# Kernel optimization log

Measured on AMD Instinct MI355X. Metric: run time of the kernel, lower is better.

## Reference

```python
import jax, jax.numpy as jnp
import numpy as np

HEADS = 4
LOCAL_CTX = 8  # local_attn_ctx (stride)


def _strided_transpose(x, n_ctx, local_ctx):
    # [B, n_ctx, E] -> reshape [B, n_ctx//local, local, E] -> swap -> [B, n_ctx, E]
    B, _, E = x.shape
    bT = n_ctx // local_ctx
    return x.reshape(B, bT, local_ctx, E).transpose(0, 2, 1, 3).reshape(B, n_ctx, E)


def _strided_untranspose(a, n_ctx, local_ctx):
    B, _, E = a.shape
    bT = n_ctx // local_ctx
    return a.reshape(B, local_ctx, bT, E).transpose(0, 2, 1, 3).reshape(B, n_ctx, E)


def setup_inputs() -> dict:
    key = jax.random.key(0)
    ks = jax.random.split(key, 6)
    B, T, E = 2048, 64, 256
    value = jax.random.normal(ks[0], (B, T, E), dtype=jnp.float32)
    k_in = jax.random.normal(ks[1], (B, T, E), dtype=jnp.float32)
    query = jax.random.normal(ks[2], (B, T, E), dtype=jnp.float32)
    mask = jnp.ones((B, T), dtype=jnp.int32)  # unused by the block
    W_ff = jax.random.normal(ks[3], (256, T * E), dtype=jnp.float32) * (1.0 / np.sqrt(T * E))
    b_ff = jax.random.normal(ks[4], (256,), dtype=jnp.float32) * 0.01
    return {"value": value, "key": k_in, "query": query, "mask": mask, "W_ff": W_ff, "b_ff": b_ff}


def reference(value, key, query, mask, W_ff, b_ff):
    B, n_ctx, E = query.shape
    # strided transpose of q, k, v
    q = _strided_transpose(query, n_ctx, LOCAL_CTX)
    k = _strided_transpose(key, n_ctx, LOCAL_CTX)
    v = _strided_transpose(value, n_ctx, LOCAL_CTX)
    scale = 1.0 / np.sqrt(E // HEADS)  # n_state = embd // heads
    w = jax.nn.softmax(jnp.einsum('bqe,bke->bqk', q, k) * scale, axis=-1)
    a = jnp.einsum('bqk,bke->bqe', w, v)
    attention = _strided_untranspose(a, n_ctx, LOCAL_CTX)
    # residual + dropout (eval-mode identity)
    x = attention + query
    # flatten-linear + ReLU
    out = jax.nn.relu(x.reshape(B, n_ctx * E) @ W_ff.T + b_ff)
    return (out, attention)
```

## Files before the change

### kernel.cpp

```cpp
#include <hip/hip_runtime.h>
#include <stdint.h>

typedef __attribute__((ext_vector_type(8))) short s16x8;
typedef __attribute__((ext_vector_type(8))) _Float16 h16x8;
typedef __attribute__((ext_vector_type(4))) float f32x4;

__device__ __forceinline__ unsigned short f2h_bits(float f) {
  union { _Float16 h; unsigned short u; } cv;
  cv.h = (_Float16)f;
  return cv.u;
}
__device__ __forceinline__ f32x4 mfma16h(h16x8 a, h16x8 b, f32x4 c) {
  return __builtin_amdgcn_mfma_f32_16x16x32_f16(a, b, c, 0, 0, 0);
}

typedef const unsigned int __attribute__((address_space(1)))* as1_u32p;
typedef unsigned int __attribute__((address_space(3)))* as3_u32p;
__device__ __forceinline__ void async_ld16(const void* g, void* l) {
  __builtin_amdgcn_global_load_lds((as1_u32p)g, (as3_u32p)l, 16, 0, 0);
}

__device__ __forceinline__ void stage_kq(char* buf, const float* Kb, int qi,
                                         int w, int lane) {
#pragma unroll
  for (int i = 0; i < 4; ++i) {
    int seg = w * 4 + i;
    int row = seg * 4 + (lane >> 4);
    int sg = (lane & 15) ^ (row & 7);
    async_ld16(Kb + row * 256 + qi * 64 + sg * 4, buf + seg * 1024);
  }
}

__device__ __forceinline__ void qk_quarter(const char* buf, const float* Qb, int qi,
                                           int w, int n, int q, f32x4* accS) {
#pragma unroll
  for (int kkl = 0; kkl < 2; ++kkl) {
    const float* qsrc = Qb + (16 * w + n) * 256 + qi * 64 + kkl * 32 + q * 8;
    float4 q0 = *(const float4*)qsrc;
    float4 q1 = *(const float4*)(qsrc + 4);
    h16x8 qh;
    qh[0] = (_Float16)q0.x; qh[1] = (_Float16)q0.y;
    qh[2] = (_Float16)q0.z; qh[3] = (_Float16)q0.w;
    qh[4] = (_Float16)q1.x; qh[5] = (_Float16)q1.y;
    qh[6] = (_Float16)q1.z; qh[7] = (_Float16)q1.w;
    const int g = kkl * 8 + q * 2;
#pragma unroll
    for (int c = 0; c < 4; ++c) {
      int row = 16 * c + n;
      int s = row & 7;
      float4 k0 = *(const float4*)(buf + row * 256 + ((g ^ s) * 16));
      float4 k1 = *(const float4*)(buf + row * 256 + (((g + 1) ^ s) * 16));
      h16x8 kh;
      kh[0] = (_Float16)k0.x; kh[1] = (_Float16)k0.y;
      kh[2] = (_Float16)k0.z; kh[3] = (_Float16)k0.w;
      kh[4] = (_Float16)k1.x; kh[5] = (_Float16)k1.y;
      kh[6] = (_Float16)k1.z; kh[7] = (_Float16)k1.w;
      accS[c] = mfma16h(qh, kh, accS[c]);
    }
  }
}

__device__ __forceinline__ void write_vq(char* base, int e, int tg, const float2* g) {
  s16x8 lo, hi;
#pragma unroll
  for (int j = 0; j < 8; ++j) {
    lo[j] = (short)f2h_bits(g[j].x);
    hi[j] = (short)f2h_bits(g[j].y);
  }
  int sw = ((e >> 1) & 7) << 4;
  *(s16x8*)(base + e * 128 + ((16 * tg) ^ sw)) = lo;
  *(s16x8*)(base + (e + 1) * 128 + ((16 * tg) ^ sw)) = hi;
}

__global__ __launch_bounds__(256, 2) void attn_kernel(
    const float* __restrict__ Vg, const float* __restrict__ Kg,
    const float* __restrict__ Qg, float* __restrict__ attn_out,
    unsigned short* __restrict__ xb ) {
  __shared__ __align__(16) char smem[65536];
  char* b0 = smem;
  char* b1 = smem + 16384;
  char* Vt = smem + 32768;
  char* PLB = smem;

  const int b = blockIdx.x;
  const int tid = threadIdx.x;
  const int lane = tid & 63;
  const int w = tid >> 6;
  const int n = lane & 15;
  const int q = lane >> 4;

  const float* Qb = Qg + (size_t)b * 64 * 256;
  const float* Kb = Kg + (size_t)b * 64 * 256;
  const float* Vb = Vg + (size_t)b * 64 * 256;

  const int ep2 = (tid & 31) * 2;
  const int tg = tid >> 5;

  f32x4 accS[4];
#pragma unroll
  for (int c = 0; c < 4; ++c) accS[c] = f32x4{0.f, 0.f, 0.f, 0.f};

  stage_kq(b0, Kb, 0, w, lane);
  stage_kq(b1, Kb, 1, w, lane);
  float2 g0[8], g1[8];
#pragma unroll
  for (int j = 0; j < 8; ++j) g0[j] = *(const float2*)(Vb + (tg * 8 + j) * 256 + 0 + ep2);
#pragma unroll
  for (int j = 0; j < 8; ++j) g1[j] = *(const float2*)(Vb + (tg * 8 + j) * 256 + 64 + ep2);
  __syncthreads();

  write_vq(Vt, 0 + ep2, tg, g0);
  write_vq(Vt, 64 + ep2, tg, g1);
  float2 g2[8], g3[8];
#pragma unroll
  for (int j = 0; j < 8; ++j) g2[j] = *(const float2*)(Vb + (tg * 8 + j) * 256 + 128 + ep2);
#pragma unroll
  for (int j = 0; j < 8; ++j) g3[j] = *(const float2*)(Vb + (tg * 8 + j) * 256 + 192 + ep2);

  qk_quarter(b0, Qb, 0, w, n, q, accS);
  __syncthreads();
  stage_kq(b0, Kb, 2, w, lane);
  qk_quarter(b1, Qb, 1, w, n, q, accS);
  __syncthreads();
  stage_kq(b1, Kb, 3, w, lane);
  write_vq(Vt, 128 + ep2, tg, g2);
  write_vq(Vt, 192 + ep2, tg, g3);
  qk_quarter(b0, Qb, 2, w, n, q, accS);
  __syncthreads();
  qk_quarter(b1, Qb, 3, w, n, q, accS);

  const float scale = 0.125f;
  float p[4][4];
#pragma unroll
  for (int r = 0; r < 4; ++r) {
    float m = -1e30f;
#pragma unroll
    for (int c = 0; c < 4; ++c) m = fmaxf(m, accS[c][r]);
#pragma unroll
    for (int mk = 1; mk < 16; mk <<= 1) m = fmaxf(m, __shfl_xor(m, mk, 64));
    float s = 0.f;
#pragma unroll
    for (int c = 0; c < 4; ++c) {
      float e = __expf((accS[c][r] - m) * scale);
      p[c][r] = e;
      s += e;
    }
#pragma unroll
    for (int mk = 1; mk < 16; mk <<= 1) s += __shfl_xor(s, mk, 64);
    float inv = 1.0f / s;
#pragma unroll
    for (int c = 0; c < 4; ++c) p[c][r] *= inv;
  }

#pragma unroll
  for (int r = 0; r < 4; ++r) {
    int row = 16 * w + 4 * q + r;
    int sw = (row & 7) << 4;
#pragma unroll
    for (int c = 0; c < 4; ++c)
      *(unsigned short*)(PLB + row * 128 + ((2 * (16 * c + n)) ^ sw)) =
          f2h_bits(p[c][r]);
  }

  __syncthreads();

  f32x4 accA[4];
#pragma unroll
  for (int qi = 0; qi < 4; ++qi) {
#pragma unroll
    for (int c = 0; c < 4; ++c) accA[c] = f32x4{0.f, 0.f, 0.f, 0.f};
    __builtin_amdgcn_s_setprio(1);
#pragma unroll
    for (int ks = 0; ks < 2; ++ks) {
      const int cb = (ks * 32 + q * 8) * 2;
      h16x8 af = *(const h16x8*)(PLB + (16 * w + n) * 128 + (cb ^ ((n & 7) << 4)));
#pragma unroll
      for (int c = 0; c < 4; ++c) {
        int row = qi * 64 + 16 * c + n;
        h16x8 bf = *(const h16x8*)(Vt + row * 128 + (cb ^ (((row >> 1) & 7) << 4)));
        accA[c] = mfma16h(af, bf, accA[c]);
      }
    }
    __builtin_amdgcn_s_setprio(0);

#pragma unroll
    for (int r = 0; r < 4; ++r) {
      int t = 16 * w + 4 * q + r;
      const float* qrow = Qb + t * 256 + qi * 64;
      size_t base = ((size_t)b * 64 + t) * 256 + qi * 64;
#pragma unroll
      for (int c = 0; c < 4; ++c) {
        int e = 16 * c + n;
        float aval = accA[c][r];
        attn_out[base + e] = aval;
        if (xb) xb[base + e] = f2h_bits(aval + qrow[e]);
      }
    }
  }
}

__global__ __launch_bounds__(256) void w2b_kernel(const float* __restrict__ W,
                                                  unsigned short* __restrict__ Wb) {
  int i = blockIdx.x * 256 + threadIdx.x;
  float4 v = ((const float4*)W)[i];
  ushort4 o;
  o.x = f2h_bits(v.x); o.y = f2h_bits(v.y); o.z = f2h_bits(v.z); o.w = f2h_bits(v.w);
  ((ushort4*)Wb)[i] = o;
}

template <bool USE_XB>
__global__ __launch_bounds__(256) void ff_kernel(
    const unsigned short* __restrict__ xb, const float* __restrict__ attn,
    const float* __restrict__ query, const unsigned short* __restrict__ Wb,
    float* __restrict__ part, int kchunk) {
  __shared__ __align__(16) unsigned short As[64 * 72];
  __shared__ __align__(16) unsigned short Bs[64 * 72];
  const int tid = threadIdx.x;
  const int lane = tid & 63, w = tid >> 6, n = lane & 15, q = lane >> 4;
  const int m0 = blockIdx.x * 64;
  const int n0 = blockIdx.y * 64;
  const int k0 = blockIdx.z * kchunk;

  f32x4 acc[4];
#pragma unroll
  for (int c = 0; c < 4; ++c) acc[c] = f32x4{0.f, 0.f, 0.f, 0.f};

  const int srow = tid >> 3;
  const int scol = (tid & 7) * 8;

  for (int kk = 0; kk < kchunk; kk += 64) {
#pragma unroll
    for (int rr = 0; rr < 2; ++rr) {
      int row = rr * 32 + srow;
      size_t ga = (size_t)(m0 + row) * 16384 + k0 + kk + scol;
      if (USE_XB) {
        *(uint4*)(As + row * 72 + scol) = *(const uint4*)(xb + ga);
      } else {
        float4 a0 = *(const float4*)(attn + ga);
        float4 a1 = *(const float4*)(attn + ga + 4);
        float4 q0 = *(const float4*)(query + ga);
        float4 q1 = *(const float4*)(query + ga + 4);
        ushort4 h0, h1;
        h0.x = f2h_bits(a0.x + q0.x); h0.y = f2h_bits(a0.y + q0.y);
        h0.z = f2h_bits(a0.z + q0.z); h0.w = f2h_bits(a0.w + q0.w);
        h1.x = f2h_bits(a1.x + q1.x); h1.y = f2h_bits(a1.y + q1.y);
        h1.z = f2h_bits(a1.z + q1.z); h1.w = f2h_bits(a1.w + q1.w);
        *(ushort4*)(As + row * 72 + scol) = h0;
        *(ushort4*)(As + row * 72 + scol + 4) = h1;
      }
      size_t gw = (size_t)(n0 + row) * 16384 + k0 + kk + scol;
      *(uint4*)(Bs + row * 72 + scol) = *(const uint4*)(Wb + gw);
    }
    __syncthreads();
#pragma unroll
    for (int ks = 0; ks < 2; ++ks) {
      const int colb = ks * 32 + q * 8;
      h16x8 af = *(const h16x8*)(As + (16 * w + n) * 72 + colb);
#pragma unroll
      for (int c = 0; c < 4; ++c) {
        h16x8 bf = *(const h16x8*)(Bs + (16 * c + n) * 72 + colb);
        acc[c] = mfma16h(af, bf, acc[c]);
      }
    }
    __syncthreads();
  }
#pragma unroll
  for (int r = 0; r < 4; ++r) {
    int m = m0 + 16 * w + 4 * q + r;
#pragma unroll
    for (int c = 0; c < 4; ++c) {
      int nn = n0 + 16 * c + n;
      part[((size_t)blockIdx.z * 2048 + m) * 256 + nn] = acc[c][r];
    }
  }
}

__global__ __launch_bounds__(256) void relu_kernel(const float* __restrict__ part,
                                                   const float* __restrict__ bias,
                                                   float* __restrict__ out, int KS) {
  int idx = blockIdx.x * 256 + threadIdx.x;
  float s = bias[idx & 255];
  for (int ks = 0; ks < KS; ++ks) s += part[(size_t)ks * 2048 * 256 + idx];
  out[idx] = fmaxf(s, 0.f);
}

extern "C" void kernel_launch(void* const* d_in, const int* in_sizes, int n_in,
                              void* d_out, int out_size, void* d_ws, size_t ws_size,
                              hipStream_t stream) {
  const float* value = (const float*)d_in[0];
  const float* key   = (const float*)d_in[1];
  const float* query = (const float*)d_in[2];
  const float* W_ff  = (const float*)d_in[4];
  const float* b_ff  = (const float*)d_in[5];

  float* out  = (float*)d_out;
  float* attn = out + (size_t)2048 * 256;

  const int KS = 4;
  const size_t wb_bytes   = (size_t)256 * 16384 * 2;
  const size_t part_bytes = (size_t)KS * 2048 * 256 * 4;
  const size_t xb_bytes   = (size_t)2048 * 64 * 256 * 2;
  unsigned short* Wb = (unsigned short*)d_ws;
  float* part = (float*)((char*)d_ws + wb_bytes);
  bool use_xb = ws_size >= wb_bytes + part_bytes + xb_bytes;
  unsigned short* xb =
      use_xb ? (unsigned short*)((char*)d_ws + wb_bytes + part_bytes) : nullptr;

  w2b_kernel<<<4096, 256, 0, stream>>>(W_ff, Wb);
  attn_kernel<<<2048, 256, 0, stream>>>(value, key, query, attn, xb);
  dim3 gb(32, 4, KS);
  if (use_xb)
    ff_kernel<true><<<gb, 256, 0, stream>>>(xb, nullptr, nullptr, Wb, part, 16384 / KS);
  else
    ff_kernel<false><<<gb, 256, 0, stream>>>(nullptr, attn, query, Wb, part, 16384 / KS);
  relu_kernel<<<2048, 256, 0, stream>>>(part, b_ff, out, KS);
}
```

Before: 280.3 us.

## Split fused attention kernel into QK-softmax and PV kernels via global P buffer

Splits the single attention kernel into a QK+softmax kernel that writes fp16 probabilities in MFMA fragment order to a workspace buffer, and a PV kernel that reloads them and stages V in LDS. K is now read straight from global memory into registers instead of through async LDS double-buffering. The aim is lower LDS use and register pressure per kernel, giving higher occupancy and simpler scheduling. In exchange it adds an extra launch, a 16 MB global round trip for P, a second read of Q in the PV kernel, and it drops the overlap of V loads with QK compute.

```diff
diff --git a/kernel.cpp b/kernel.cpp
--- a/kernel.cpp
+++ b/kernel.cpp
@@ -13,74 +13,17 @@
 __device__ __forceinline__ f32x4 mfma16h(h16x8 a, h16x8 b, f32x4 c) {
   return __builtin_amdgcn_mfma_f32_16x16x32_f16(a, b, c, 0, 0, 0);
 }
-
-typedef const unsigned int __attribute__((address_space(1)))* as1_u32p;
-typedef unsigned int __attribute__((address_space(3)))* as3_u32p;
-__device__ __forceinline__ void async_ld16(const void* g, void* l) {
-  __builtin_amdgcn_global_load_lds((as1_u32p)g, (as3_u32p)l, 16, 0, 0);
-}
-
-__device__ __forceinline__ void stage_kq(char* buf, const float* Kb, int qi,
-                                         int w, int lane) {
-#pragma unroll
-  for (int i = 0; i < 4; ++i) {
-    int seg = w * 4 + i;
-    int row = seg * 4 + (lane >> 4);
-    int sg = (lane & 15) ^ (row & 7);
-    async_ld16(Kb + row * 256 + qi * 64 + sg * 4, buf + seg * 1024);
-  }
-}
-
-__device__ __forceinline__ void qk_quarter(const char* buf, const float* Qb, int qi,
-                                           int w, int n, int q, f32x4* accS) {
-#pragma unroll
-  for (int kkl = 0; kkl < 2; ++kkl) {
-    const float* qsrc = Qb + (16 * w + n) * 256 + qi * 64 + kkl * 32 + q * 8;
-    float4 q0 = *(const float4*)qsrc;
-    float4 q1 = *(const float4*)(qsrc + 4);
-    h16x8 qh;
-    qh[0] = (_Float16)q0.x; qh[1] = (_Float16)q0.y;
-    qh[2] = (_Float16)q0.z; qh[3] = (_Float16)q0.w;
-    qh[4] = (_Float16)q1.x; qh[5] = (_Float16)q1.y;
-    qh[6] = (_Float16)q1.z; qh[7] = (_Float16)q1.w;
-    const int g = kkl * 8 + q * 2;
-#pragma unroll
-    for (int c = 0; c < 4; ++c) {
-      int row = 16 * c + n;
-      int s = row & 7;
-      float4 k0 = *(const float4*)(buf + row * 256 + ((g ^ s) * 16));
-      float4 k1 = *(const float4*)(buf + row * 256 + (((g + 1) ^ s) * 16));
-      h16x8 kh;
-      kh[0] = (_Float16)k0.x; kh[1] = (_Float16)k0.y;
-      kh[2] = (_Float16)k0.z; kh[3] = (_Float16)k0.w;
-      kh[4] = (_Float16)k1.x; kh[5] = (_Float16)k1.y;
-      kh[6] = (_Float16)k1.z; kh[7] = (_Float16)k1.w;
-      accS[c] = mfma16h(qh, kh, accS[c]);
-    }
-  }
-}
-
-__device__ __forceinline__ void write_vq(char* base, int e, int tg, const float2* g) {
-  s16x8 lo, hi;
-#pragma unroll
-  for (int j = 0; j < 8; ++j) {
-    lo[j] = (short)f2h_bits(g[j].x);
-    hi[j] = (short)f2h_bits(g[j].y);
-  }
-  int sw = ((e >> 1) & 7) << 4;
-  *(s16x8*)(base + e * 128 + ((16 * tg) ^ sw)) = lo;
-  *(s16x8*)(base + (e + 1) * 128 + ((16 * tg) ^ sw)) = hi;
-}
-
-__global__ __launch_bounds__(256, 2) void attn_kernel(
-    const float* __restrict__ Vg, const float* __restrict__ Kg,
-    const float* __restrict__ Qg, float* __restrict__ attn_out,
-    unsigned short* __restrict__ xb ) {
-  __shared__ __align__(16) char smem[65536];
-  char* b0 = smem;
-  char* b1 = smem + 16384;
-  char* Vt = smem + 32768;
-  char* PLB = smem;
+__device__ __forceinline__ h16x8 cvt8(float4 x, float4 y) {
+  h16x8 r;
+  r[0] = (_Float16)x.x; r[1] = (_Float16)x.y; r[2] = (_Float16)x.z; r[3] = (_Float16)x.w;
+  r[4] = (_Float16)y.x; r[5] = (_Float16)y.y; r[6] = (_Float16)y.z; r[7] = (_Float16)y.w;
+  return r;
+}
+
+__global__ __launch_bounds__(256) void qk_kernel(
+    const float* __restrict__ Kg, const float* __restrict__ Qg,
+    unsigned short* __restrict__ Pg) {
+  __shared__ __align__(16) char PL[8192];
 
   const int b = blockIdx.x;
   const int tid = threadIdx.x;
@@ -91,43 +34,32 @@
 
   const float* Qb = Qg + (size_t)b * 64 * 256;
   const float* Kb = Kg + (size_t)b * 64 * 256;
-  const float* Vb = Vg + (size_t)b * 64 * 256;
-
-  const int ep2 = (tid & 31) * 2;
-  const int tg = tid >> 5;
 
   f32x4 accS[4];
 #pragma unroll
   for (int c = 0; c < 4; ++c) accS[c] = f32x4{0.f, 0.f, 0.f, 0.f};
 
-  stage_kq(b0, Kb, 0, w, lane);
-  stage_kq(b1, Kb, 1, w, lane);
-  float2 g0[8], g1[8];
-#pragma unroll
-  for (int j = 0; j < 8; ++j) g0[j] = *(const float2*)(Vb + (tg * 8 + j) * 256 + 0 + ep2);
-#pragma unroll
-  for (int j = 0; j < 8; ++j) g1[j] = *(const float2*)(Vb + (tg * 8 + j) * 256 + 64 + ep2);
-  __syncthreads();
-
-  write_vq(Vt, 0 + ep2, tg, g0);
-  write_vq(Vt, 64 + ep2, tg, g1);
-  float2 g2[8], g3[8];
-#pragma unroll
-  for (int j = 0; j < 8; ++j) g2[j] = *(const float2*)(Vb + (tg * 8 + j) * 256 + 128 + ep2);
-#pragma unroll
-  for (int j = 0; j < 8; ++j) g3[j] = *(const float2*)(Vb + (tg * 8 + j) * 256 + 192 + ep2);
-
-  qk_quarter(b0, Qb, 0, w, n, q, accS);
-  __syncthreads();
-  stage_kq(b0, Kb, 2, w, lane);
-  qk_quarter(b1, Qb, 1, w, n, q, accS);
-  __syncthreads();
-  stage_kq(b1, Kb, 3, w, lane);
-  write_vq(Vt, 128 + ep2, tg, g2);
-  write_vq(Vt, 192 + ep2, tg, g3);
-  qk_quarter(b0, Qb, 2, w, n, q, accS);
-  __syncthreads();
-  qk_quarter(b1, Qb, 3, w, n, q, accS);
+#pragma unroll
+  for (int ph = 0; ph < 2; ++ph) {
+#pragma unroll
+    for (int kk = 0; kk < 4; ++kk) {
+      const int cb = ph * 128 + kk * 32 + q * 8;
+      const float* qsrc = Qb + (16 * w + n) * 256 + cb;
+      float4 q0 = *(const float4*)qsrc;
+      float4 q1 = *(const float4*)(qsrc + 4);
+      float4 k0[4], k1[4];
+#pragma unroll
+      for (int c = 0; c < 4; ++c) {
+        const float* ksrc = Kb + (16 * c + n) * 256 + cb;
+        k0[c] = *(const float4*)ksrc;
+        k1[c] = *(const float4*)(ksrc + 4);
+      }
+      h16x8 qh = cvt8(q0, q1);
+#pragma unroll
+      for (int c = 0; c < 4; ++c)
+        accS[c] = mfma16h(qh, cvt8(k0[c], k1[c]), accS[c]);
+    }
+  }
 
   const float scale = 0.125f;
   float p[4][4];
@@ -158,10 +90,64 @@
     int sw = (row & 7) << 4;
 #pragma unroll
     for (int c = 0; c < 4; ++c)
-      *(unsigned short*)(PLB + row * 128 + ((2 * (16 * c + n)) ^ sw)) =
+      *(unsigned short*)(PL + row * 128 + ((2 * (16 * c + n)) ^ sw)) =
           f2h_bits(p[c][r]);
   }
-
+#pragma unroll
+  for (int ks = 0; ks < 2; ++ks) {
+    const int cb = (ks * 32 + q * 8) * 2;
+    s16x8 af = *(const s16x8*)(PL + (16 * w + n) * 128 + (cb ^ ((n & 7) << 4)));
+    *(s16x8*)(Pg + ((size_t)(b * 4 + w) * 2 + ks) * 512 + lane * 8) = af;
+  }
+}
+
+__device__ __forceinline__ void write_vq(char* base, int e, int tg, const float2* g) {
+  s16x8 lo, hi;
+#pragma unroll
+  for (int j = 0; j < 8; ++j) {
+    lo[j] = (short)f2h_bits(g[j].x);
+    hi[j] = (short)f2h_bits(g[j].y);
+  }
+  int sw = ((e >> 1) & 7) << 4;
+  *(s16x8*)(base + e * 128 + ((16 * tg) ^ sw)) = lo;
+  *(s16x8*)(base + (e + 1) * 128 + ((16 * tg) ^ sw)) = hi;
+}
+
+__global__ __launch_bounds__(256) void pv_kernel(
+    const float* __restrict__ Vg, const float* __restrict__ Qg,
+    const unsigned short* __restrict__ Pg, float* __restrict__ attn_out,
+    unsigned short* __restrict__ xb ) {
+  __shared__ __align__(16) char Vt[32768];
+
+  const int b = blockIdx.x;
+  const int tid = threadIdx.x;
+  const int lane = tid & 63;
+  const int w = tid >> 6;
+  const int n = lane & 15;
+  const int q = lane >> 4;
+
+  const float* Vb = Vg + (size_t)b * 64 * 256;
+  const float* Qb = Qg + (size_t)b * 64 * 256;
+
+  const int ep2 = (tid & 31) * 2;
+  const int tg = tid >> 5;
+
+  float2 g0[8], g1[8], g2[8], g3[8];
+#pragma unroll
+  for (int j = 0; j < 8; ++j) g0[j] = *(const float2*)(Vb + (tg * 8 + j) * 256 + 0 + ep2);
+#pragma unroll
+  for (int j = 0; j < 8; ++j) g1[j] = *(const float2*)(Vb + (tg * 8 + j) * 256 + 64 + ep2);
+#pragma unroll
+  for (int j = 0; j < 8; ++j) g2[j] = *(const float2*)(Vb + (tg * 8 + j) * 256 + 128 + ep2);
+#pragma unroll
+  for (int j = 0; j < 8; ++j) g3[j] = *(const float2*)(Vb + (tg * 8 + j) * 256 + 192 + ep2);
+  h16x8 af0 = *(const h16x8*)(Pg + ((size_t)(b * 4 + w) * 2 + 0) * 512 + lane * 8);
+  h16x8 af1 = *(const h16x8*)(Pg + ((size_t)(b * 4 + w) * 2 + 1) * 512 + lane * 8);
+
+  write_vq(Vt, 0 + ep2, tg, g0);
+  write_vq(Vt, 64 + ep2, tg, g1);
+  write_vq(Vt, 128 + ep2, tg, g2);
+  write_vq(Vt, 192 + ep2, tg, g3);
   __syncthreads();
 
   f32x4 accA[4];
@@ -173,7 +159,7 @@
 #pragma unroll
     for (int ks = 0; ks < 2; ++ks) {
       const int cb = (ks * 32 + q * 8) * 2;
-      h16x8 af = *(const h16x8*)(PLB + (16 * w + n) * 128 + (cb ^ ((n & 7) << 4)));
+      h16x8 af = ks ? af1 : af0;
 #pragma unroll
       for (int c = 0; c < 4; ++c) {
         int row = qi * 64 + 16 * c + n;
@@ -299,18 +285,22 @@
   const int KS = 4;
   const size_t wb_bytes   = (size_t)256 * 16384 * 2;
   const size_t part_bytes = (size_t)KS * 2048 * 256 * 4;
+  const size_t p_bytes    = (size_t)2048 * 64 * 64 * 2;
   const size_t xb_bytes   = (size_t)2048 * 64 * 256 * 2;
   unsigned short* Wb = (unsigned short*)d_ws;
   float* part = (float*)((char*)d_ws + wb_bytes);
-  bool use_xb = ws_size >= wb_bytes + part_bytes + xb_bytes;
-  unsigned short* xb =
-      use_xb ? (unsigned short*)((char*)d_ws + wb_bytes + part_bytes) : nullptr;
+  unsigned short* Pg = (unsigned short*)((char*)d_ws + wb_bytes + part_bytes);
+  bool use_xb = ws_size >= wb_bytes + part_bytes + p_bytes + xb_bytes;
+  unsigned short* xbp =
+      use_xb ? (unsigned short*)((char*)d_ws + wb_bytes + part_bytes + p_bytes)
+             : nullptr;
 
   w2b_kernel<<<4096, 256, 0, stream>>>(W_ff, Wb);
-  attn_kernel<<<2048, 256, 0, stream>>>(value, key, query, attn, xb);
+  qk_kernel<<<2048, 256, 0, stream>>>(key, query, Pg);
+  pv_kernel<<<2048, 256, 0, stream>>>(value, query, Pg, attn, xbp);
   dim3 gb(32, 4, KS);
   if (use_xb)
-    ff_kernel<true><<<gb, 256, 0, stream>>>(xb, nullptr, nullptr, Wb, part, 16384 / KS);
+    ff_kernel<true><<<gb, 256, 0, stream>>>(xbp, nullptr, nullptr, Wb, part, 16384 / KS);
   else
     ff_kernel<false><<<gb, 256, 0, stream>>>(nullptr, attn, query, Wb, part, 16384 / KS);
   relu_kernel<<<2048, 256, 0, stream>>>(part, b_ff, out, KS);
```

After: 307.7 us. +9.8%, slower.
